# Kernel optimization log

Measured on AMD Instinct MI355X. Metric: run time of the kernel, lower is better.

The kernel has to match this reference:

```python
import jax, jax.numpy as jnp
import numpy as np

# SLAYER SRM-alpha neuron parameters
THETA = 10.0      # spike threshold
TAU_SR = 10.0     # synaptic response time constant
TAU_REF = 1.0     # refractory time constant
SCALE_REF = 2.0   # refractory scale
TS = 1.0          # simulation step
K_SRM = 100       # srm kernel truncation (exp(1-t/10) negligible past t=100)
K_REF = 32        # refractory kernel truncation


def _srm_kernel():
    t = jnp.arange(K_SRM, dtype=jnp.float32) * TS
    return (t / TAU_SR) * jnp.exp(1.0 - t / TAU_SR)


def _ref_kernel():
    # refractory response at offsets 1..K_REF after a spike (value at 0 is 0)
    t = jnp.arange(1, K_REF + 1, dtype=jnp.float32) * TS
    return -SCALE_REF * THETA * (t / TAU_REF) * jnp.exp(1.0 - t / TAU_REF)


def psp(x):
    """Causal temporal convolution with the SRM alpha kernel along last axis."""
    T = x.shape[-1]
    xf = x.reshape(-1, 1, T)
    w = _srm_kernel()[::-1][None, None, :]  # flip -> true convolution
    out = jax.lax.conv_general_dilated(xf, w, window_strides=(1,), padding=[(K_SRM - 1, 0)])
    return out.reshape(x.shape)


def _spike_fn(u):
    return (u >= THETA).astype(u.dtype)


def spike_dynamics(u):
    """Sequential threshold + refractory recurrence over last (time) axis."""
    ref = _ref_kernel().astype(u.dtype)
    uT = jnp.moveaxis(u, -1, 0)                       # (T, ...)
    carry0 = jnp.zeros(uT.shape[1:] + (K_REF,), u.dtype)  # pending refractory additions

    def step(carry, ut):
        v = ut + carry[..., 0]
        s = _spike_fn(v)
        nxt = jnp.concatenate([carry[..., 1:], jnp.zeros_like(carry[..., :1])], axis=-1)
        nxt = nxt + s[..., None] * ref
        return nxt, s

    _, sT = jax.lax.scan(step, carry0, uT)
    return jnp.moveaxis(sT, 0, -1)


def dense(x, w):
    # SLAYER dense: bias-free linear over channel dim, per (h,w,t)
    return jnp.einsum('nchwt,oc->nohwt', x, w)


def setup_inputs() -> dict:
    key = jax.random.key(0)
    ks = jax.random.split(key, 5)
    N, C, T, H, O = 64, 156, 500, 512, 20
    spike_input = (jax.random.uniform(ks[0], (N, C, 1, 1, T)) < 0.05).astype(jnp.float32)
    w_fc1 = jax.random.normal(ks[1], (H, C), jnp.float32) * (8.0 / np.sqrt(C))
    w_fc2 = jax.random.normal(ks[2], (O, H), jnp.float32) * (8.0 / np.sqrt(H))
    w_loc1 = jax.random.normal(ks[3], (H, T), jnp.float32) * (8.0 / np.sqrt(T))
    w_loc2 = jax.random.normal(ks[4], (O, H), jnp.float32) * (8.0 / np.sqrt(H))
    inner_outer = [21, 15, 16, 23, 27, 24, 17, 6, 9, 12, 20, 29, 33, 34, 31, 28, 22, 14,
                   10, 1, 2, 7, 18, 30, 37, 39, 38, 32, 19, 8, 3, 4, 11, 25, 35, 36, 26, 13, 5]
    perm = []
    for i in inner_outer:
        perm += [2 * i - 2, 2 * i - 1]
    for i in inner_outer:
        perm += [2 * i - 2 + 78, 2 * i - 1 + 78]
    perm = jnp.asarray(perm, dtype=jnp.int32)
    return {'spike_input': spike_input, 'w_fc1': w_fc1, 'w_fc2': w_fc2,
            'w_loc1': w_loc1, 'w_loc2': w_loc2, 'perm': perm}


def reference(spike_input, w_fc1, w_fc2, w_loc1, w_loc2, perm):
    # temporal path
    s1 = spike_dynamics(psp(dense(spike_input, w_fc1)))          # (N,H,1,1,T)
    spike_output = spike_dynamics(psp(dense(s1, w_fc2)))         # (N,O,1,1,T)
    # location path: swap channel<->time, permute taxels, treat taxel axis as 'time'
    xt = jnp.swapaxes(spike_input, 1, 4)                          # (N,T,1,1,C)
    xt = xt[..., perm]
    l1 = spike_dynamics(psp(dense(xt, w_loc1)))                   # (N,H,1,1,C)
    location_spike_output = spike_dynamics(psp(dense(l1, w_loc2)))  # (N,O,1,1,C)
    return jnp.concatenate([spike_output, location_spike_output], axis=4)
```

## Files before the change

### kernel.cpp

```cpp
#include <hip/hip_runtime.h>
#include <stdint.h>

#define THETA 10.0

struct RC {
    double trs, r2s, g1, c100, c101;
    double trr, r2r, a1c, a33, a34;
};
__device__ __forceinline__ RC make_rc() {
    RC c;
    double rs = exp(-0.1); c.trs = 2.0 * rs; c.r2s = rs * rs;
    c.g1 = 0.1 * exp(0.9); c.c100 = -10.0 * exp(-9.0); c.c101 = 9.9 * exp(-9.1);
    double rr = exp(-1.0); c.trr = 2.0 * rr; c.r2r = rr * rr;
    c.a1c = -20.0; c.a33 = 660.0 * exp(-32.0); c.a34 = -640.0 * exp(-33.0);
    return c;
}
__device__ __forceinline__ int rstep(const RC& c, double din, double ta, double tb,
                                     double& y1, double& y2, double& R1, double& R2,
                                     uint64_t& mask) {
    double y = c.trs * y1 - c.r2s * y2 + c.g1 * din + c.c100 * ta + c.c101 * tb;
    y2 = y1; y1 = y;
    double R = c.trr * R1 - c.r2r * R2 + c.a1c * (double)(mask & 1ull)
             + c.a33 * (double)((mask >> 32) & 1ull)
             + c.a34 * (double)((mask >> 33) & 1ull);
    R2 = R1; R1 = R;
    int s = (y + R >= THETA) ? 1 : 0;
    mask = (mask << 1) | (uint64_t)s;
    return s;
}

__global__ __launch_bounds__(256) void k_prep(const float* __restrict__ x,
                                              const float* __restrict__ w_fc1,
                                              const float* __restrict__ w_loc1,
                                              uint64_t* __restrict__ xb,
                                              uint64_t* __restrict__ xbT,
                                              float* __restrict__ w1t,
                                              float* __restrict__ wl1t) {
    __shared__ float shf[156 * 65];
    int b = blockIdx.x, tid = threadIdx.x;
    if (b < 512) {
        int n = b >> 3, wd = b & 7;
        int t0 = wd * 64;
        for (int e = tid; e < 156 * 64; e += 256) {
            int c = e >> 6, tt = e & 63;
            int t = t0 + tt;
            shf[c * 65 + tt] = (t < 500) ? x[(size_t)n * 78000 + (size_t)c * 500 + t] : 0.0f;
        }
        __syncthreads();
        int wv = tid >> 6, lane = tid & 63;
        for (int c = wv; c < 156; c += 4) {
            uint64_t bal = __ballot(shf[c * 65 + lane] != 0.0f);
            if (lane == 0) xbT[((size_t)n * 156 + c) * 8 + wd] = bal;
        }
        if (tid < 64) {
            int t = t0 + tid;
            if (t < 500) {
                uint64_t w0 = 0, w1 = 0, w2 = 0;
#pragma unroll
                for (int c = 0; c < 156; ++c) {
                    uint64_t bit = (shf[c * 65 + tid] != 0.0f) ? 1ull : 0ull;
                    if (c < 64) w0 |= bit << c;
                    else if (c < 128) w1 |= bit << (c - 64);
                    else w2 |= bit << (c - 128);
                }
                size_t o = ((size_t)n * 500 + t) * 4;
                xb[o] = w0; xb[o + 1] = w1; xb[o + 2] = w2; xb[o + 3] = 0;
            }
        }
    } else {
        const float* src; float* dst; int C, k0, h0;
        if (b < 536) { int tk = b - 512; src = w_fc1; dst = w1t; C = 156;
                       k0 = (tk >> 3) * 64; h0 = (tk & 7) * 64; }
        else         { int tk = b - 536; src = w_loc1; dst = wl1t; C = 500;
                       k0 = (tk >> 3) * 64; h0 = (tk & 7) * 64; }
#pragma unroll
        for (int p = 0; p < 16; ++p) {
            int e = tid + p * 256;
            int hh = e >> 6, kk = e & 63;
            int k = k0 + kk;
            shf[hh * 65 + kk] = (k < C) ? src[(size_t)(h0 + hh) * C + k] : 0.0f;
        }
        __syncthreads();
#pragma unroll
        for (int p = 0; p < 16; ++p) {
            int e = tid + p * 256;
            int hh = e & 63, kk = e >> 6;
            int k = k0 + kk;
            if (k < C) dst[(size_t)k * 512 + h0 + hh] = shf[hh * 65 + kk];
        }
    }
}

__device__ __forceinline__ void sdenseA_body2(const uint64_t* __restrict__ xb,
                                              const float* __restrict__ w1t,
                                              double* __restrict__ d1w,
                                              int w, int tl, int n, int h) {
    const uint64_t* mb = xb + ((size_t)n * 500 + w * 125 + tl) * 4;
    uint64_t m0 = mb[0], m1 = mb[1], m2 = mb[2];
    double a0 = 0.0, a1 = 0.0, a2 = 0.0;
    double b0 = 0.0, b1 = 0.0, b2 = 0.0;
    while (m0) {
        int bb = __builtin_ctzll(m0);
        const float* p = w1t + (size_t)bb * 512;
        a0 += (double)p[h]; b0 += (double)p[h + 256];
        m0 &= m0 - 1;
    }
    while (m1) {
        int bb = __builtin_ctzll(m1);
        const float* p = w1t + (size_t)(64 + bb) * 512;
        a1 += (double)p[h]; b1 += (double)p[h + 256];
        m1 &= m1 - 1;
    }
    while (m2) {
        int bb = __builtin_ctzll(m2);
        const float* p = w1t + (size_t)(128 + bb) * 512;
        a2 += (double)p[h]; b2 += (double)p[h + 256];
        m2 &= m2 - 1;
    }
    size_t base = (size_t)tl * 32768 + n * 512;
    d1w[base + h] = (a0 + a1) + a2;
    d1w[base + h + 256] = (b0 + b1) + b2;
}

__device__ __forceinline__ void sdenseB_body2(const uint64_t* __restrict__ xbT,
                                              const float* __restrict__ wl1t,
                                              double* __restrict__ e,
                                              int c, int n, int h) {
    const uint64_t* mb = xbT + ((size_t)n * 156 + c) * 8;
    double da = 0.0, db = 0.0;
#pragma unroll
    for (int wd = 0; wd < 8; ++wd) {
        uint64_t mw = mb[wd];
        const float* wbase = wl1t + (size_t)wd * 64 * 512;
        while (mw) {
            int bb = __builtin_ctzll(mw);
            const float* p = wbase + (size_t)bb * 512;
            da += (double)p[h]; db += (double)p[h + 256];
            mw &= mw - 1;
        }
    }
    size_t base = ((size_t)n * 156 + c) * 512;
    e[base + h] = da;
    e[base + h + 256] = db;
}

__global__ __launch_bounds__(256) void k_sdenseA(const uint64_t* __restrict__ xb,
                                                 const float* __restrict__ w1t,
                                                 double* __restrict__ d1w, int w) {
    sdenseA_body2(xb, w1t, d1w, w, blockIdx.x, blockIdx.y, threadIdx.x);
}

__global__ __launch_bounds__(256) void k_sdense0(const uint64_t* __restrict__ xb,
                                                 const float* __restrict__ w1t,
                                                 double* __restrict__ d1w,
                                                 const uint64_t* __restrict__ xbT,
                                                 const float* __restrict__ wl1t,
                                                 double* __restrict__ e) {
    int b = blockIdx.x, tid = threadIdx.x;
    if (b < 8000) {
        int tl = b % 125, n = b / 125;
        sdenseA_body2(xb, w1t, d1w, 0, tl, n, tid);
    } else {
        int idx = b - 8000;
        int c = idx % 156, n = idx / 156;
        sdenseB_body2(xbT, wl1t, e, c, n, tid);
    }
}

__device__ __forceinline__ void rscanA_body(const double* __restrict__ cur,
                                            const double* __restrict__ prev,
                                            uint64_t* __restrict__ s1w,
                                            double* stY1, double* stY2,
                                            double* stR1, double* stR2,
                                            double* stDp, uint64_t* stM,
                                            int w, int lane, int blk,
                                            double (*ring)[64]) {
    int gid = blk * 64 + lane;
    int n = gid >> 9, word = (gid >> 6) & 7;
    RC rc = make_rc();
    int t0g = w * 125;
    double y1, y2, R1, R2, dp; uint64_t mask;
    if (w == 0) { y1 = y2 = R1 = R2 = dp = 0.0; mask = 0; }
    else {
        y1 = stY1[gid]; y2 = stY2[gid]; R1 = stR1[gid]; R2 = stR2[gid];
        dp = stDp[gid]; mask = stM[gid];
#pragma unroll 4
        for (int k = 0; k < 101; ++k)
            ring[(t0g - 101 + k) & 127][lane] = prev[(size_t)(24 + k) * 32768 + gid];
    }
    double curv[12], nxt[12];
#pragma unroll
    for (int i = 0; i < 12; ++i) curv[i] = cur[(size_t)i * 32768 + gid];
    for (int ch = 0; ch < 10; ++ch) {
        int b0 = ch * 12;
#pragma unroll
        for (int i = 0; i < 12; ++i) {
            int l = b0 + 12 + i;
            nxt[i] = (l < 125) ? cur[(size_t)l * 32768 + gid] : 0.0;
        }
#pragma unroll
        for (int i = 0; i < 12; ++i) ring[(t0g + b0 + i) & 127][lane] = curv[i];
#pragma unroll
        for (int i = 0; i < 12; ++i) {
            int tg = t0g + b0 + i;
            double ta = (tg >= 100) ? ring[(tg - 100) & 127][lane] : 0.0;
            double tb = (tg >= 101) ? ring[(tg - 101) & 127][lane] : 0.0;
            int s = rstep(rc, (i == 0) ? dp : curv[i - 1], ta, tb, y1, y2, R1, R2, mask);
            uint64_t bal = __ballot(s != 0);
            if (lane == 0) s1w[((size_t)n * 500 + tg) * 8 + word] = bal;
        }
        dp = curv[11];
#pragma unroll
        for (int i = 0; i < 12; ++i) curv[i] = nxt[i];
    }
#pragma unroll
    for (int i = 0; i < 5; ++i) ring[(t0g + 120 + i) & 127][lane] = curv[i];
#pragma unroll
    for (int i = 0; i < 5; ++i) {
        int tg = t0g + 120 + i;
        double ta = ring[(tg - 100) & 127][lane];
        double tb = ring[(tg - 101) & 127][lane];
        int s = rstep(rc, (i == 0) ? dp : curv[i - 1], ta, tb, y1, y2, R1, R2, mask);
        uint64_t bal = __ballot(s != 0);
        if (lane == 0) s1w[((size_t)n * 500 + tg) * 8 + word] = bal;
    }
    dp = curv[4];
    stY1[gid] = y1; stY2[gid] = y2; stR1[gid] = R1; stR2[gid] = R2;
    stDp[gid] = dp; stM[gid] = mask;
}

__device__ __forceinline__ void rscanB_body(const double* __restrict__ e,
                                            const int* pl,
                                            uint64_t* __restrict__ s1bw,
                                            int lane, int blk,
                                            double (*ring)[64]) {
    int gid = blk * 64 + lane;
    int n = gid >> 9, h = gid & 511, word = (gid >> 6) & 7;
    const double* en = e + (size_t)n * 156 * 512;
    RC rc = make_rc();
    double y1 = 0.0, y2 = 0.0, R1 = 0.0, R2 = 0.0, dp = 0.0; uint64_t mask = 0;
    double curv[12], nxt[12];
#pragma unroll
    for (int i = 0; i < 12; ++i) curv[i] = en[(size_t)pl[i] * 512 + h];
    for (int ch = 0; ch < 13; ++ch) {
        int b0 = ch * 12;
        if (ch < 12) {
#pragma unroll
            for (int i = 0; i < 12; ++i) nxt[i] = en[(size_t)pl[b0 + 12 + i] * 512 + h];
        }
#pragma unroll
        for (int i = 0; i < 12; ++i) ring[(b0 + i) & 127][lane] = curv[i];
#pragma unroll
        for (int i = 0; i < 12; ++i) {
            int j = b0 + i;
            double ta = (j >= 100) ? ring[(j - 100) & 127][lane] : 0.0;
            double tb = (j >= 101) ? ring[(j - 101) & 127][lane] : 0.0;
            int s = rstep(rc, (i == 0) ? dp : curv[i - 1], ta, tb, y1, y2, R1, R2, mask);
            uint64_t bal = __ballot(s != 0);
            if (lane == 0) s1bw[((size_t)n * 156 + j) * 8 + word] = bal;
        }
        dp = curv[11];
#pragma unroll
        for (int i = 0; i < 12; ++i) curv[i] = nxt[i];
    }
}

__global__ __launch_bounds__(64) void k_rscanA(const double* __restrict__ cur,
                                               const double* __restrict__ prev,
                                               uint64_t* __restrict__ s1w,
                                               double* stY1, double* stY2,
                                               double* stR1, double* stR2,
                                               double* stDp, uint64_t* stM, int w) {
    __shared__ double ring[128][64];
    rscanA_body(cur, prev, s1w, stY1, stY2, stR1, stR2, stDp, stM,
                w, threadIdx.x, blockIdx.x, ring);
}

__global__ __launch_bounds__(64) void k_rscan0(const double* __restrict__ cur,
                                               uint64_t* __restrict__ s1w,
                                               double* stY1, double* stY2,
                                               double* stR1, double* stR2,
                                               double* stDp, uint64_t* stM,
                                               const double* __restrict__ e,
                                               const int* __restrict__ perm,
                                               uint64_t* __restrict__ s1bw) {
    __shared__ double ring[128][64];
    __shared__ int pl[156];
    int b = blockIdx.x, lane = threadIdx.x;
    if (b < 512) {
        rscanA_body(cur, cur, s1w, stY1, stY2, stR1, stR2, stDp, stM,
                    0, lane, b, ring);
    } else {
        for (int i = lane; i < 156; i += 64) pl[i] = perm[i];
        __syncthreads();
        rscanB_body(e, pl, s1bw, lane, b - 512, ring);
    }
}

__global__ __launch_bounds__(256) void k_dense2m(const uint64_t* __restrict__ s1w,
                                                 const uint64_t* __restrict__ s1bw,
                                                 const float* __restrict__ w_fc2,
                                                 const float* __restrict__ w_loc2,
                                                 double* __restrict__ a2,
                                                 double* __restrict__ a2b) {
    __shared__ float wt[512 * 20];
    int b = blockIdx.x, tid = threadIdx.x;
    int isA = (b < 125);
    const float* w = isA ? w_fc2 : w_loc2;
    const uint64_t* sw = isA ? s1w : s1bw;
    double* a = isA ? a2 : a2b;
    int T = isA ? 500 : 156;
    int gid = (isA ? b : (b - 125)) * 256 + tid;
    for (int e = tid; e < 512 * 20; e += 256) { int o = e / 512, hh = e % 512; wt[hh * 20 + o] = w[e]; }
    __syncthreads();
    if (gid >= 64 * T) return;
    int n = gid / T, t = gid - n * T;
    const uint64_t* r = sw + ((size_t)n * T + t) * 8;
    uint64_t wbuf[8];
#pragma unroll
    for (int wd = 0; wd < 8; ++wd) wbuf[wd] = r[wd];
    double acc[20];
#pragma unroll
    for (int o = 0; o < 20; ++o) acc[o] = 0.0;
#pragma unroll
    for (int wd = 0; wd < 8; ++wd) {
        uint64_t mw = wbuf[wd];
        while (mw) {
            int bb = __builtin_ctzll(mw);
            const float* wp = wt + (wd * 64 + bb) * 20;
#pragma unroll
            for (int o = 0; o < 20; ++o) acc[o] += (double)wp[o];
            mw &= mw - 1;
        }
    }
#pragma unroll
    for (int o = 0; o < 20; ++o) a[(size_t)t * 1280 + n * 20 + o] = acc[o];
}

template<int NFULL, int TAIL>
__device__ __forceinline__ void ring_scan(const double* __restrict__ a, int row,
                                          double (*ring)[64],
                                          uint32_t (*bits)[64], int lane) {
    RC rc = make_rc();
    double y1 = 0.0, y2 = 0.0, R1 = 0.0, R2 = 0.0, dp = 0.0; uint64_t mask = 0;
    double cur[24], nxt[24];
#pragma unroll
    for (int i = 0; i < 24; ++i) cur[i] = a[(size_t)i * 1280 + row];
    for (int ch = 0; ch < NFULL; ++ch) {
        int t0 = ch * 24;
        if (ch + 1 < NFULL) {
#pragma unroll
            for (int i = 0; i < 24; ++i) nxt[i] = a[(size_t)(t0 + 24 + i) * 1280 + row];
        } else if (TAIL > 0) {
#pragma unroll
            for (int i = 0; i < 24; ++i)
                nxt[i] = (i < TAIL) ? a[(size_t)(t0 + 24 + i) * 1280 + row] : 0.0;
        }
#pragma unroll
        for (int i = 0; i < 24; ++i) ring[(t0 + i) & 127][lane] = cur[i];
        double tap[25];
#pragma unroll
        for (int i = 0; i < 25; ++i) {
            int l = t0 + i - 101;
            tap[i] = (l >= 0) ? ring[l & 127][lane] : 0.0;
        }
        uint32_t sp = 0;
#pragma unroll
        for (int i = 0; i < 24; ++i) {
            int s = rstep(rc, (i == 0) ? dp : cur[i - 1], tap[i + 1], tap[i],
                          y1, y2, R1, R2, mask);
            sp |= (uint32_t)s << i;
        }
        dp = cur[23];
        bits[ch][lane] = sp;
#pragma unroll
        for (int i = 0; i < 24; ++i) cur[i] = nxt[i];
    }
    if (TAIL > 0) {
        int t0 = NFULL * 24;
#pragma unroll
        for (int i = 0; i < 24; ++i) if (i < TAIL) ring[(t0 + i) & 127][lane] = cur[i];
        double tap[25];
#pragma unroll
        for (int i = 0; i < 25; ++i) {
            if (i > TAIL) break;
            int l = t0 + i - 101;
            tap[i] = (l >= 0) ? ring[l & 127][lane] : 0.0;
        }
        uint32_t sp = 0;
#pragma unroll
        for (int i = 0; i < 24; ++i) {
            if (i >= TAIL) break;
            int s = rstep(rc, (i == 0) ? dp : cur[i - 1], tap[i + 1], tap[i],
                          y1, y2, R1, R2, mask);
            sp |= (uint32_t)s << i;
        }
        bits[NFULL][lane] = sp;
    }
}

template<int T>
__device__ __forceinline__ void expand_bits(uint32_t (*bits)[64],
                                            float* __restrict__ out,
                                            int row0, int coff, int lane) {
    for (int r = 0; r < 64; ++r) {
        float* orow = out + (size_t)(row0 + r) * 656 + coff;
        for (int c0 = 0; c0 < T; c0 += 64) {
            int c = c0 + lane;
            if (c < T) orow[c] = (float)((bits[c / 24][r] >> (c % 24)) & 1);
        }
    }
}

__global__ __launch_bounds__(64) void k_out3(const double* __restrict__ a2,
                                             const double* __restrict__ a2b,
                                             float* __restrict__ out) {
    __shared__ double ring[128][64];
    __shared__ uint32_t bits[21][64];
    int b = blockIdx.x, lane = threadIdx.x;
    if (b < 20) {
        int row0 = b * 64;
        ring_scan<20, 20>(a2, row0 + lane, ring, bits, lane);
        expand_bits<500>(bits, out, row0, 0, lane);
    } else {
        int row0 = (b - 20) * 64;
        ring_scan<6, 12>(a2b, row0 + lane, ring, bits, lane);
        expand_bits<156>(bits, out, row0, 500, lane);
    }
}

extern "C" void kernel_launch(void* const* d_in, const int* in_sizes, int n_in,
                              void* d_out, int out_size, void* d_ws, size_t ws_size,
                              hipStream_t stream) {
    const float* x      = (const float*)d_in[0];
    const float* w_fc1  = (const float*)d_in[1];
    const float* w_fc2  = (const float*)d_in[2];
    const float* w_loc1 = (const float*)d_in[3];
    const float* w_loc2 = (const float*)d_in[4];
    const int*   perm   = (const int*)d_in[5];
    float* out = (float*)d_out;
    char* ws = (char*)d_ws;
    (void)ws_size; (void)in_sizes; (void)n_in; (void)out_size;

    double*   d1b0 = (double*)(ws + 0);
    double*   d1b1 = (double*)(ws + 32768000);
    double*   a2   = (double*)(ws + 40894464);
    double*   a2b  = (double*)(ws + 46014464);
    double*   e    = (double*)(ws + 65536000);
    uint64_t* s1w  = (uint64_t*)(ws + 106430464);
    uint64_t* s1bw = (uint64_t*)(ws + 108990464);
    uint64_t* xb   = (uint64_t*)(ws + 109629440);
    uint64_t* xbT  = (uint64_t*)(ws + 110653440);
    float*    w1t  = (float*)(ws + 111292416);
    float*    wl1t = (float*)(ws + 111611904);
    double*   stY1 = (double*)(ws + 112635904);
    double*   stY2 = (double*)(ws + 112898048);
    double*   stR1 = (double*)(ws + 113160192);
    double*   stR2 = (double*)(ws + 113422336);
    double*   stDp = (double*)(ws + 113684480);
    uint64_t* stM  = (uint64_t*)(ws + 113946624);

    k_prep<<<600, 256, 0, stream>>>(x, w_fc1, w_loc1, xb, xbT, w1t, wl1t);
    k_sdense0<<<17984, 256, 0, stream>>>(xb, w1t, d1b0, xbT, wl1t, e);
    k_rscan0<<<1024, 64, 0, stream>>>(d1b0, s1w, stY1, stY2, stR1, stR2, stDp, stM, e, perm, s1bw);
    dim3 ga(125, 64);
    for (int w = 1; w < 4; ++w) {
        double* cur  = (w & 1) ? d1b1 : d1b0;
        double* prev = (w & 1) ? d1b0 : d1b1;
        k_sdenseA<<<ga, 256, 0, stream>>>(xb, w1t, cur, w);
        k_rscanA<<<512, 64, 0, stream>>>(cur, prev, s1w, stY1, stY2, stR1, stR2, stDp, stM, w);
    }
    k_dense2m<<<164, 256, 0, stream>>>(s1w, s1bw, w_fc2, w_loc2, a2, a2b);
    k_out3<<<40, 64, 0, stream>>>(a2, a2b, out);
}
```

Measured before the change: 403.5 us.

## Compute full-length dense in one pass and scan all timesteps in one kernel

When the workspace is large enough, the dense layer-1 output for all 500 timesteps is materialized at once, and a single recurrence scan kernel processes the whole sequence. This replaces the four-window loop of dense and scan launches, which saved and restored state between windows. Dense threads now each compute 4 hidden outputs with 128-thread blocks instead of 2 outputs with 256 threads. The cost is a much larger workspace, and a fallback path keeps the old windowed schedule when the workspace is small.

```diff
diff --git a/kernel.cpp b/kernel.cpp
--- a/kernel.cpp
+++ b/kernel.cpp
@@ -91,79 +91,104 @@
     }
 }
 
-__device__ __forceinline__ void sdenseA_body2(const uint64_t* __restrict__ xb,
+__device__ __forceinline__ void sdenseA_body4(const uint64_t* __restrict__ xb,
                                               const float* __restrict__ w1t,
                                               double* __restrict__ d1w,
-                                              int w, int tl, int n, int h) {
-    const uint64_t* mb = xb + ((size_t)n * 500 + w * 125 + tl) * 4;
+                                              int tl, int n, int h) {
+    const uint64_t* mb = xb + ((size_t)n * 500 + tl) * 4;
     uint64_t m0 = mb[0], m1 = mb[1], m2 = mb[2];
-    double a0 = 0.0, a1 = 0.0, a2 = 0.0;
-    double b0 = 0.0, b1 = 0.0, b2 = 0.0;
+    double acc[4][3];
+#pragma unroll
+    for (int q = 0; q < 4; ++q) { acc[q][0] = 0.0; acc[q][1] = 0.0; acc[q][2] = 0.0; }
     while (m0) {
         int bb = __builtin_ctzll(m0);
-        const float* p = w1t + (size_t)bb * 512;
-        a0 += (double)p[h]; b0 += (double)p[h + 256];
+        const float* p = w1t + (size_t)bb * 512 + h;
+#pragma unroll
+        for (int q = 0; q < 4; ++q) acc[q][0] += (double)p[q * 128];
         m0 &= m0 - 1;
     }
     while (m1) {
         int bb = __builtin_ctzll(m1);
-        const float* p = w1t + (size_t)(64 + bb) * 512;
-        a1 += (double)p[h]; b1 += (double)p[h + 256];
+        const float* p = w1t + (size_t)(64 + bb) * 512 + h;
+#pragma unroll
+        for (int q = 0; q < 4; ++q) acc[q][1] += (double)p[q * 128];
         m1 &= m1 - 1;
     }
     while (m2) {
         int bb = __builtin_ctzll(m2);
-        const float* p = w1t + (size_t)(128 + bb) * 512;
-        a2 += (double)p[h]; b2 += (double)p[h + 256];
+        const float* p = w1t + (size_t)(128 + bb) * 512 + h;
+#pragma unroll
+        for (int q = 0; q < 4; ++q) acc[q][2] += (double)p[q * 128];
         m2 &= m2 - 1;
     }
     size_t base = (size_t)tl * 32768 + n * 512;
-    d1w[base + h] = (a0 + a1) + a2;
-    d1w[base + h + 256] = (b0 + b1) + b2;
-}
-
-__device__ __forceinline__ void sdenseB_body2(const uint64_t* __restrict__ xbT,
+#pragma unroll
+    for (int q = 0; q < 4; ++q)
+        d1w[base + h + q * 128] = (acc[q][0] + acc[q][1]) + acc[q][2];
+}
+
+__device__ __forceinline__ void sdenseB_body4(const uint64_t* __restrict__ xbT,
                                               const float* __restrict__ wl1t,
                                               double* __restrict__ e,
                                               int c, int n, int h) {
     const uint64_t* mb = xbT + ((size_t)n * 156 + c) * 8;
-    double da = 0.0, db = 0.0;
+    double acc[4];
+#pragma unroll
+    for (int q = 0; q < 4; ++q) acc[q] = 0.0;
 #pragma unroll
     for (int wd = 0; wd < 8; ++wd) {
         uint64_t mw = mb[wd];
-        const float* wbase = wl1t + (size_t)wd * 64 * 512;
+        const float* wbase = wl1t + (size_t)wd * 64 * 512 + h;
         while (mw) {
             int bb = __builtin_ctzll(mw);
             const float* p = wbase + (size_t)bb * 512;
-            da += (double)p[h]; db += (double)p[h + 256];
+#pragma unroll
+            for (int q = 0; q < 4; ++q) acc[q] += (double)p[q * 128];
             mw &= mw - 1;
         }
     }
     size_t base = ((size_t)n * 156 + c) * 512;
-    e[base + h] = da;
-    e[base + h + 256] = db;
-}
-
-__global__ __launch_bounds__(256) void k_sdenseA(const uint64_t* __restrict__ xb,
-                                                 const float* __restrict__ w1t,
-                                                 double* __restrict__ d1w, int w) {
-    sdenseA_body2(xb, w1t, d1w, w, blockIdx.x, blockIdx.y, threadIdx.x);
-}
-
-__global__ __launch_bounds__(256) void k_sdense0(const uint64_t* __restrict__ xb,
-                                                 const float* __restrict__ w1t,
-                                                 double* __restrict__ d1w,
-                                                 const uint64_t* __restrict__ xbT,
-                                                 const float* __restrict__ wl1t,
-                                                 double* __restrict__ e) {
-    int b = blockIdx.x, tid = threadIdx.x;
+#pragma unroll
+    for (int q = 0; q < 4; ++q) e[base + h + q * 128] = acc[q];
+}
+
+__global__ __launch_bounds__(128) void k_sdense_full(const uint64_t* __restrict__ xb,
+                                                     const float* __restrict__ w1t,
+                                                     double* __restrict__ d1,
+                                                     const uint64_t* __restrict__ xbT,
+                                                     const float* __restrict__ wl1t,
+                                                     double* __restrict__ e) {
+    int b = blockIdx.x, h = threadIdx.x;
+    if (b < 32000) {
+        int tl = b % 500, n = b / 500;
+        sdenseA_body4(xb, w1t, d1, tl, n, h);
+    } else {
+        int idx = b - 32000;
+        int c = idx % 156, n = idx / 156;
+        sdenseB_body4(xbT, wl1t, e, c, n, h);
+    }
+}
+
+__global__ __launch_bounds__(128) void k_sdenseA_fb(const uint64_t* __restrict__ xb,
+                                                    const float* __restrict__ w1t,
+                                                    double* __restrict__ d1w, int w) {
+    sdenseA_body4(xb, w1t, d1w - (size_t)w * 125 * 32768, w * 125 + blockIdx.x,
+                  blockIdx.y, threadIdx.x);
+}
+__global__ __launch_bounds__(128) void k_sdense0_fb(const uint64_t* __restrict__ xb,
+                                                    const float* __restrict__ w1t,
+                                                    double* __restrict__ d1w,
+                                                    const uint64_t* __restrict__ xbT,
+                                                    const float* __restrict__ wl1t,
+                                                    double* __restrict__ e) {
+    int b = blockIdx.x, h = threadIdx.x;
     if (b < 8000) {
         int tl = b % 125, n = b / 125;
-        sdenseA_body2(xb, w1t, d1w, 0, tl, n, tid);
+        sdenseA_body4(xb, w1t, d1w, tl, n, h);
     } else {
         int idx = b - 8000;
         int c = idx % 156, n = idx / 156;
-        sdenseB_body2(xbT, wl1t, e, c, n, tid);
+        sdenseB_body4(xbT, wl1t, e, c, n, h);
     }
 }
 
@@ -265,6 +290,62 @@
     }
 }
 
+__global__ __launch_bounds__(64) void k_rscan_full(const double* __restrict__ d1,
+                                                   uint64_t* __restrict__ s1w,
+                                                   const double* __restrict__ e,
+                                                   const int* __restrict__ perm,
+                                                   uint64_t* __restrict__ s1bw) {
+    __shared__ double ring[128][64];
+    __shared__ int pl[156];
+    int b = blockIdx.x, lane = threadIdx.x;
+    if (b < 512) {
+        int gid = b * 64 + lane;
+        int n = gid >> 9, word = (gid >> 6) & 7;
+        RC rc = make_rc();
+        double y1 = 0.0, y2 = 0.0, R1 = 0.0, R2 = 0.0, dp = 0.0; uint64_t mask = 0;
+        double curv[12], nxt[12];
+#pragma unroll
+        for (int i = 0; i < 12; ++i) curv[i] = d1[(size_t)i * 32768 + gid];
+        for (int ch = 0; ch < 41; ++ch) {
+            int b0 = ch * 12;
+#pragma unroll
+            for (int i = 0; i < 12; ++i) {
+                int l = b0 + 12 + i;
+                nxt[i] = (l < 500) ? d1[(size_t)l * 32768 + gid] : 0.0;
+            }
+#pragma unroll
+            for (int i = 0; i < 12; ++i) ring[(b0 + i) & 127][lane] = curv[i];
+#pragma unroll
+            for (int i = 0; i < 12; ++i) {
+                int tg = b0 + i;
+                double ta = (tg >= 100) ? ring[(tg - 100) & 127][lane] : 0.0;
+                double tb = (tg >= 101) ? ring[(tg - 101) & 127][lane] : 0.0;
+                int s = rstep(rc, (i == 0) ? dp : curv[i - 1], ta, tb, y1, y2, R1, R2, mask);
+                uint64_t bal = __ballot(s != 0);
+                if (lane == 0) s1w[((size_t)n * 500 + tg) * 8 + word] = bal;
+            }
+            dp = curv[11];
+#pragma unroll
+            for (int i = 0; i < 12; ++i) curv[i] = nxt[i];
+        }
+#pragma unroll
+        for (int i = 0; i < 8; ++i) ring[(492 + i) & 127][lane] = curv[i];
+#pragma unroll
+        for (int i = 0; i < 8; ++i) {
+            int tg = 492 + i;
+            double ta = ring[(tg - 100) & 127][lane];
+            double tb = ring[(tg - 101) & 127][lane];
+            int s = rstep(rc, (i == 0) ? dp : curv[i - 1], ta, tb, y1, y2, R1, R2, mask);
+            uint64_t bal = __ballot(s != 0);
+            if (lane == 0) s1w[((size_t)n * 500 + tg) * 8 + word] = bal;
+        }
+    } else {
+        for (int i = lane; i < 156; i += 64) pl[i] = perm[i];
+        __syncthreads();
+        rscanB_body(e, pl, s1bw, lane, b - 512, ring);
+    }
+}
+
 __global__ __launch_bounds__(64) void k_rscanA(const double* __restrict__ cur,
                                                const double* __restrict__ prev,
                                                uint64_t* __restrict__ s1w,
@@ -275,7 +356,6 @@
     rscanA_body(cur, prev, s1w, stY1, stY2, stR1, stR2, stDp, stM,
                 w, threadIdx.x, blockIdx.x, ring);
 }
-
 __global__ __launch_bounds__(64) void k_rscan0(const double* __restrict__ cur,
                                                uint64_t* __restrict__ s1w,
                                                double* stY1, double* stY2,
@@ -440,7 +520,28 @@
     const int*   perm   = (const int*)d_in[5];
     float* out = (float*)d_out;
     char* ws = (char*)d_ws;
-    (void)ws_size; (void)in_sizes; (void)n_in; (void)out_size;
+    (void)in_sizes; (void)n_in; (void)out_size;
+
+    const size_t NEED_MAIN = 184889344;
+    if (ws_size >= NEED_MAIN) {
+        double*   d1   = (double*)(ws + 0);
+        double*   e    = (double*)(ws + 131072000);
+        double*   a2   = (double*)(ws + 171966464);
+        double*   a2b  = (double*)(ws + 177086464);
+        uint64_t* s1w  = (uint64_t*)(ws + 178683904);
+        uint64_t* s1bw = (uint64_t*)(ws + 181243904);
+        uint64_t* xb   = (uint64_t*)(ws + 181882880);
+        uint64_t* xbT  = (uint64_t*)(ws + 182906880);
+        float*    w1t  = (float*)(ws + 183545856);
+        float*    wl1t = (float*)(ws + 183865344);
+
+        k_prep<<<600, 256, 0, stream>>>(x, w_fc1, w_loc1, xb, xbT, w1t, wl1t);
+        k_sdense_full<<<41984, 128, 0, stream>>>(xb, w1t, d1, xbT, wl1t, e);
+        k_rscan_full<<<1024, 64, 0, stream>>>(d1, s1w, e, perm, s1bw);
+        k_dense2m<<<164, 256, 0, stream>>>(s1w, s1bw, w_fc2, w_loc2, a2, a2b);
+        k_out3<<<40, 64, 0, stream>>>(a2, a2b, out);
+        return;
+    }
 
     double*   d1b0 = (double*)(ws + 0);
     double*   d1b1 = (double*)(ws + 32768000);
@@ -461,13 +562,13 @@
     uint64_t* stM  = (uint64_t*)(ws + 113946624);
 
     k_prep<<<600, 256, 0, stream>>>(x, w_fc1, w_loc1, xb, xbT, w1t, wl1t);
-    k_sdense0<<<17984, 256, 0, stream>>>(xb, w1t, d1b0, xbT, wl1t, e);
+    k_sdense0_fb<<<17984, 128, 0, stream>>>(xb, w1t, d1b0, xbT, wl1t, e);
     k_rscan0<<<1024, 64, 0, stream>>>(d1b0, s1w, stY1, stY2, stR1, stR2, stDp, stM, e, perm, s1bw);
     dim3 ga(125, 64);
     for (int w = 1; w < 4; ++w) {
         double* cur  = (w & 1) ? d1b1 : d1b0;
         double* prev = (w & 1) ? d1b0 : d1b1;
-        k_sdenseA<<<ga, 256, 0, stream>>>(xb, w1t, cur, w);
+        k_sdenseA_fb<<<ga, 128, 0, stream>>>(xb, w1t, cur, w);
         k_rscanA<<<512, 64, 0, stream>>>(cur, prev, s1w, stY1, stY2, stR1, stR2, stDp, stM, w);
     }
     k_dense2m<<<164, 256, 0, stream>>>(s1w, s1bw, w_fc2, w_loc2, a2, a2b);
```

Result: faster. 327.9 us (-18.7%).
